# Optimization experiments

Measured on AMD Instinct MI355X. Metric: run time of the kernel, lower is better.

The kernel has to match this reference:

```python
import jax, jax.numpy as jnp
import numpy as np

B, L, C, H = 1, 256, 128, 4  # batch, seq len, c_z, n_heads
D = C // H                    # head_dim = 32


def setup_inputs() -> dict:
    key = jax.random.key(0)
    ks = jax.random.split(key, 8)
    w = lambda k, shape: jax.random.normal(k, shape, jnp.float32) * 0.02
    return {
        "pair": jax.random.normal(ks[0], (B, L, L, C), jnp.float32),
        "ln_g": jnp.ones((C,), jnp.float32),
        "ln_b": jnp.zeros((C,), jnp.float32),
        "Wq": w(ks[1], (C, C)),
        "Wk": w(ks[2], (C, C)),
        "Wv": w(ks[3], (C, C)),
        "Wbias": w(ks[4], (C, H)),
        "Wo": w(ks[5], (C, C)),
        "bo": jnp.zeros((C,), jnp.float32),
        "Wg": w(ks[6], (C, C)),
        "bg": jnp.zeros((C,), jnp.float32),
    }


def reference(pair, ln_g, ln_b, Wq, Wk, Wv, Wbias, Wo, bo, Wg, bg):
    # mode == 'starting': no transpose of pair
    # LayerNorm over c_z
    mu = jnp.mean(pair, axis=-1, keepdims=True)
    var = jnp.mean(jnp.square(pair - mu), axis=-1, keepdims=True)
    z = (pair - mu) * jax.lax.rsqrt(var + 1e-5) * ln_g + ln_b

    q = (z @ Wq).reshape(B, L, L, H, D)
    k = (z @ Wk).reshape(B, L, L, H, D)
    v = (z @ Wv).reshape(B, L, L, H, D)

    # logits: [B, H, i, j, k], scaled by 1/sqrt(head_dim)
    attn = jnp.einsum('bijhd,bikhd->bhijk', q, k) * (1.0 / np.sqrt(D).astype(np.float32))
    # pairwise additive bias: bias_proj(z) -> [B, L, L, H] -> [B, H, 1, j, k]
    bias = jnp.einsum('bjkc,ch->bhjk', z, Wbias)[:, :, None, :, :]
    attn = jax.nn.softmax(attn + bias, axis=-1)

    out = jnp.einsum('bhijk,bikhd->bijhd', attn, v).reshape(B, L, L, C)
    result = pair + jax.nn.sigmoid(pair @ Wg + bg) * (out @ Wo + bo)
    return result
```

## Files before the change

kernel.cpp:

```cpp
#include <hip/hip_runtime.h>
#include <cstdint>
#include <cstddef>

#define L_ 256
#define C_ 128
#define H_ 4
#define D_ 32
#define NP_ (L_ * L_)

typedef unsigned short u16;
typedef uint32_t u32;
typedef __attribute__((ext_vector_type(8))) short bf16x8;
typedef __attribute__((ext_vector_type(4))) float f32x4;

__device__ __forceinline__ float bflo(u32 u) { union { u32 i; float f; } v; v.i = u << 16; return v.f; }
__device__ __forceinline__ float bfhi(u32 u) { union { u32 i; float f; } v; v.i = u & 0xffff0000u; return v.f; }
__device__ __forceinline__ float b2f(u16 u) { union { u32 i; float f; } v; v.i = ((u32)u) << 16; return v.f; }
__device__ __forceinline__ u16 f2b(float f) {
    u32 x = __float_as_uint(f);
    return (u16)((x + 0x7fffu + ((x >> 16) & 1u)) >> 16);
}
__device__ __forceinline__ u32 pk2(float lo, float hi) {
    return ((u32)f2b(hi) << 16) | (u32)f2b(lo);
}
__device__ __forceinline__ bf16x8 pack8(float4 a, float4 b) {
    union { u32 u[4]; bf16x8 v; } r;
    r.u[0] = pk2(a.x, a.y); r.u[1] = pk2(a.z, a.w);
    r.u[2] = pk2(b.x, b.y); r.u[3] = pk2(b.z, b.w);
    return r.v;
}

__global__ __launch_bounds__(256) void k_prep(
    const float* __restrict__ Wq, const float* __restrict__ Wk, const float* __restrict__ Wv,
    const float* __restrict__ Wo, const float* __restrict__ Wg,
    const float* __restrict__ Wbias, u16* __restrict__ Wt, float* __restrict__ WbT)
{
    __shared__ float tile[64][65];
    const int b = blockIdx.x, t = threadIdx.x;
    if (b < 20) {
        const int mat = b >> 2, tl = b & 3, tr = tl >> 1, tc = tl & 1;
        const float* W = (mat == 0) ? Wq : (mat == 1) ? Wk : (mat == 2) ? Wv : (mat == 3) ? Wo : Wg;
        const float s = (mat == 0) ? 0.17677669529663687f : 1.f;
        const int rlo = t >> 6, col = t & 63;
        #pragma unroll
        for (int m = 0; m < 16; ++m) {
            int row = m * 4 + rlo;
            tile[row][col] = W[(size_t)(tr * 64 + row) * C_ + tc * 64 + col];
        }
        __syncthreads();
        #pragma unroll
        for (int m = 0; m < 16; ++m) {
            int n = tc * 64 + m * 4 + rlo;
            int c = tr * 64 + col;
            Wt[mat * 16384 + n * C_ + c] = f2b(tile[col][m * 4 + rlo] * s);
        }
    } else {
        #pragma unroll
        for (int m = 0; m < 2; ++m) {
            int idx = m * 256 + t;
            int h = idx >> 7, c = idx & 127;
            WbT[h * C_ + c] = Wbias[c * H_ + h];
        }
    }
}

__global__ __launch_bounds__(256) void k_lnmm(
    const float* __restrict__ pair, const float* __restrict__ ln_g, const float* __restrict__ ln_b,
    const u16* __restrict__ Wt, const float* __restrict__ WbT,
    u16* __restrict__ qh, u16* __restrict__ kh, u16* __restrict__ vh,
    u16* __restrict__ biasT)
{
    __shared__ u16 zsh[64][136];

    const int t  = threadIdx.x;
    const int p0 = blockIdx.x * 64;
    const int row = t >> 2, seg = t & 3;

    float4 xv[8];
    float sum = 0.f, ss = 0.f;
    #pragma unroll
    for (int i = 0; i < 8; ++i) {
        int c = (seg + 4 * i) * 4;
        float4 x = *(const float4*)(pair + (size_t)(p0 + row) * C_ + c);
        xv[i] = x;
        sum += x.x + x.y + x.z + x.w;
        ss  += x.x * x.x + x.y * x.y + x.z * x.z + x.w * x.w;
    }
    sum += __shfl_xor(sum, 1); sum += __shfl_xor(sum, 2);
    ss  += __shfl_xor(ss, 1);  ss  += __shfl_xor(ss, 2);
    float mu  = sum * (1.0f / C_);
    float var = ss * (1.0f / C_) - mu * mu;
    float rs  = rsqrtf(fmaxf(var, 0.f) + 1e-5f);

    #pragma unroll
    for (int i = 0; i < 8; ++i) {
        int c = (seg + 4 * i) * 4;
        float4 g4 = *(const float4*)(ln_g + c);
        float4 b4 = *(const float4*)(ln_b + c);
        float4 x  = xv[i];
        float z0 = (x.x - mu) * rs * g4.x + b4.x;
        float z1 = (x.y - mu) * rs * g4.y + b4.y;
        float z2 = (x.z - mu) * rs * g4.z + b4.z;
        float z3 = (x.w - mu) * rs * g4.w + b4.w;
        *(u32*)&zsh[row][c]     = pk2(z0, z1);
        *(u32*)&zsh[row][c + 2] = pk2(z2, z3);
    }
    __syncthreads();

    const int w    = t >> 6;
    const int l15  = t & 15;
    const int quad = (t >> 4) & 3;

    bf16x8 zf[4][4];
    #pragma unroll
    for (int jt = 0; jt < 4; ++jt)
        #pragma unroll
        for (int kc = 0; kc < 4; ++kc)
            zf[jt][kc] = *(const bf16x8*)&zsh[jt * 16 + l15][kc * 32 + quad * 8];

    #pragma unroll
    for (int k = 0; k < 6; ++k) {
        const int tt = w * 6 + k;
        const int mat = tt >> 3, mt = tt & 7;
        f32x4 acc0 = {0.f,0.f,0.f,0.f}, acc1 = acc0, acc2 = acc0, acc3 = acc0;
        #pragma unroll
        for (int kc = 0; kc < 4; ++kc) {
            bf16x8 af = *(const bf16x8*)(Wt + (size_t)tt * 2048 + (size_t)l15 * 128 + kc * 32 + quad * 8);
            acc0 = __builtin_amdgcn_mfma_f32_16x16x32_bf16(af, zf[0][kc], acc0, 0, 0, 0);
            acc1 = __builtin_amdgcn_mfma_f32_16x16x32_bf16(af, zf[1][kc], acc1, 0, 0, 0);
            acc2 = __builtin_amdgcn_mfma_f32_16x16x32_bf16(af, zf[2][kc], acc2, 0, 0, 0);
            acc3 = __builtin_amdgcn_mfma_f32_16x16x32_bf16(af, zf[3][kc], acc3, 0, 0, 0);
        }
        u16* dst = (mat == 0) ? qh : (mat == 1) ? kh : vh;
        const int hh = mt >> 1;
        const int cb = (mt & 1) * 16 + quad * 4;
        f32x4 accs[4] = {acc0, acc1, acc2, acc3};
        #pragma unroll
        for (int jt = 0; jt < 4; ++jt) {
            const int p = p0 + jt * 16 + l15;
            *(uint2*)(dst + ((size_t)hh * NP_ + p) * D_ + cb) =
                make_uint2(pk2(accs[jt][0], accs[jt][1]), pk2(accs[jt][2], accs[jt][3]));
        }
    }

    {
        float a = 0.f;
        #pragma unroll
        for (int c8 = 0; c8 < C_; c8 += 8) {
            uint4 zz = *(const uint4*)&zsh[row][c8];
            float4 wb0 = *(const float4*)(WbT + seg * C_ + c8);
            float4 wb1 = *(const float4*)(WbT + seg * C_ + c8 + 4);
            a += bflo(zz.x) * wb0.x + bfhi(zz.x) * wb0.y
               + bflo(zz.y) * wb0.z + bfhi(zz.y) * wb0.w
               + bflo(zz.z) * wb1.x + bfhi(zz.z) * wb1.y
               + bflo(zz.w) * wb1.z + bfhi(zz.w) * wb1.w;
        }
        const int p = p0 + row;
        biasT[(size_t)seg * NP_ + (p & 255) * 256 + (p >> 8)] = f2b(a);
    }
}

__global__ __launch_bounds__(256) void k_attn(
    u16* __restrict__ qh, const u16* __restrict__ kh, const u16* __restrict__ vh,
    const u16* __restrict__ biasT)
{
    __shared__ u16 Vsh[D_ * 264];
    __shared__ u16 Psh[4][16][40];

    const int t = threadIdx.x;
    const int i = blockIdx.x >> 2;
    const int h = blockIdx.x & 3;
    const int w    = t >> 6;
    const int l15  = t & 15;
    const int quad = (t >> 4) & 3;
    const int jbase = w * 64;

    const u16* Kg = kh + ((size_t)h * NP_ + i * L_) * D_;
    const u16* Vg = vh + ((size_t)h * NP_ + i * L_) * D_;
    u16*       Qg = qh + ((size_t)h * NP_ + i * L_) * D_;

    #pragma unroll
    for (int jj = 0; jj < 8; ++jj) {
        int idx = t + jj * 256;
        int r = idx >> 2, sg = idx & 3;
        union { uint4 q; u16 s[8]; } u;
        u.q = *(const uint4*)(Vg + r * D_ + sg * 8);
        #pragma unroll
        for (int m = 0; m < 8; ++m) Vsh[(sg * 8 + m) * 264 + r] = u.s[m];
    }

    bf16x8 qf[4];
    #pragma unroll
    for (int jt = 0; jt < 4; ++jt)
        qf[jt] = *(const bf16x8*)(Qg + (size_t)(jbase + jt * 16 + l15) * D_ + quad * 8);

    __syncthreads();

    const f32x4 z4 = {0.f, 0.f, 0.f, 0.f};
    f32x4 oacc[4][2];
    float psum[4][4];
    #pragma unroll
    for (int jt = 0; jt < 4; ++jt) {
        oacc[jt][0] = z4; oacc[jt][1] = z4;
        #pragma unroll
        for (int r = 0; r < 4; ++r) psum[jt][r] = 0.f;
    }

    const u16* bT = biasT + (size_t)h * NP_;

    bf16x8 kb0 = *(const bf16x8*)(Kg + (size_t)l15 * D_ + quad * 8);
    bf16x8 kb1 = *(const bf16x8*)(Kg + (size_t)(16 + l15) * D_ + quad * 8);

    for (int kc = 0; kc < 8; ++kc) {
        bf16x8 nb0, nb1;
        if (kc < 7) {
            nb0 = *(const bf16x8*)(Kg + (size_t)((kc + 1) * 32 + l15) * D_ + quad * 8);
            nb1 = *(const bf16x8*)(Kg + (size_t)((kc + 1) * 32 + 16 + l15) * D_ + quad * 8);
        }
        bf16x8 vb0 = *(const bf16x8*)&Vsh[l15 * 264 + kc * 32 + quad * 8];
        bf16x8 vb1 = *(const bf16x8*)&Vsh[(16 + l15) * 264 + kc * 32 + quad * 8];

        #pragma unroll
        for (int jt = 0; jt < 4; ++jt) {
            f32x4 s0 = __builtin_amdgcn_mfma_f32_16x16x32_bf16(qf[jt], kb0, z4, 0, 0, 0);
            f32x4 s1 = __builtin_amdgcn_mfma_f32_16x16x32_bf16(qf[jt], kb1, z4, 0, 0, 0);

            const int j0 = jbase + jt * 16 + quad * 4;
            uint2 bv0 = *(const uint2*)(bT + (size_t)(kc * 32 + l15) * L_ + j0);
            uint2 bv1 = *(const uint2*)(bT + (size_t)(kc * 32 + 16 + l15) * L_ + j0);
            const u16* b0p = (const u16*)&bv0;
            const u16* b1p = (const u16*)&bv1;

            u16 (*P)[40] = Psh[w];
            float e0[4], e1[4];
            #pragma unroll
            for (int r = 0; r < 4; ++r) {
                e0[r] = __expf(s0[r] + b2f(b0p[r]));
                e1[r] = __expf(s1[r] + b2f(b1p[r]));
                psum[jt][r] += e0[r] + e1[r];
            }
            #pragma unroll
            for (int r = 0; r < 4; ++r) {
                P[quad * 4 + r][l15]      = f2b(e0[r]);
                P[quad * 4 + r][16 + l15] = f2b(e1[r]);
            }
            bf16x8 pa = *(const bf16x8*)&P[l15][quad * 8];
            oacc[jt][0] = __builtin_amdgcn_mfma_f32_16x16x32_bf16(pa, vb0, oacc[jt][0], 0, 0, 0);
            oacc[jt][1] = __builtin_amdgcn_mfma_f32_16x16x32_bf16(pa, vb1, oacc[jt][1], 0, 0, 0);
        }
        kb0 = nb0; kb1 = nb1;
    }

    float rn[4][4];
    #pragma unroll
    for (int jt = 0; jt < 4; ++jt)
        #pragma unroll
        for (int r = 0; r < 4; ++r) {
            float s = psum[jt][r];
            s += __shfl_xor(s, 1); s += __shfl_xor(s, 2);
            s += __shfl_xor(s, 4); s += __shfl_xor(s, 8);
            rn[jt][r] = 1.f / s;
        }

    #pragma unroll
    for (int jt = 0; jt < 4; ++jt) {
        #pragma unroll
        for (int r = 0; r < 4; ++r) {
            size_t rowo = (size_t)(jbase + jt * 16 + quad * 4 + r) * D_;
            Qg[rowo + l15]      = f2b(oacc[jt][0][r] * rn[jt][r]);
            Qg[rowo + 16 + l15] = f2b(oacc[jt][1][r] * rn[jt][r]);
        }
    }
}

__global__ __launch_bounds__(256) void k_out(
    const u16* __restrict__ aoh, const float* __restrict__ pair,
    const u16* __restrict__ Wt, const float* __restrict__ bo,
    const float* __restrict__ bg, float* __restrict__ out)
{
    const int t  = threadIdx.x;
    const int p0 = blockIdx.x * 128;
    const int w    = t >> 6;
    const int l15  = t & 15;
    const int quad = (t >> 4) & 3;

    bf16x8 aof[2][4], pf[2][4];
    int prow[2];
    #pragma unroll
    for (int g = 0; g < 2; ++g) {
        prow[g] = p0 + w * 32 + g * 16 + l15;
        #pragma unroll
        for (int kc = 0; kc < 4; ++kc) {
            aof[g][kc] = *(const bf16x8*)(aoh + ((size_t)kc * NP_ + prow[g]) * D_ + quad * 8);
            const float* pp = pair + (size_t)prow[g] * C_ + kc * 32 + quad * 8;
            pf[g][kc] = pack8(*(const float4*)pp, *(const float4*)(pp + 4));
        }
    }

    const u16* WoT = Wt + 3 * 16384;
    const u16* WgT = Wt + 4 * 16384;

    #pragma unroll
    for (int nt = 0; nt < 8; ++nt) {
        f32x4 accO0 = {0.f,0.f,0.f,0.f}, accO1 = accO0, accG0 = accO0, accG1 = accO0;
        #pragma unroll
        for (int kc = 0; kc < 4; ++kc) {
            bf16x8 awo = *(const bf16x8*)(WoT + (size_t)(nt * 16 + l15) * 128 + kc * 32 + quad * 8);
            bf16x8 awg = *(const bf16x8*)(WgT + (size_t)(nt * 16 + l15) * 128 + kc * 32 + quad * 8);
            accO0 = __builtin_amdgcn_mfma_f32_16x16x32_bf16(awo, aof[0][kc], accO0, 0, 0, 0);
            accO1 = __builtin_amdgcn_mfma_f32_16x16x32_bf16(awo, aof[1][kc], accO1, 0, 0, 0);
            accG0 = __builtin_amdgcn_mfma_f32_16x16x32_bf16(awg, pf[0][kc],  accG0, 0, 0, 0);
            accG1 = __builtin_amdgcn_mfma_f32_16x16x32_bf16(awg, pf[1][kc],  accG1, 0, 0, 0);
        }
        const int ch = nt * 16 + quad * 4;
        float4 bo4 = *(const float4*)(bo + ch);
        float4 bg4 = *(const float4*)(bg + ch);
        f32x4 aO[2] = {accO0, accO1}, aG[2] = {accG0, accG1};
        #pragma unroll
        for (int g = 0; g < 2; ++g) {
            float4 pr = *(const float4*)(pair + (size_t)prow[g] * C_ + ch);
            float4 r;
            r.x = pr.x + (1.f / (1.f + __expf(-(aG[g][0] + bg4.x)))) * (aO[g][0] + bo4.x);
            r.y = pr.y + (1.f / (1.f + __expf(-(aG[g][1] + bg4.y)))) * (aO[g][1] + bo4.y);
            r.z = pr.z + (1.f / (1.f + __expf(-(aG[g][2] + bg4.z)))) * (aO[g][2] + bo4.z);
            r.w = pr.w + (1.f / (1.f + __expf(-(aG[g][3] + bg4.w)))) * (aO[g][3] + bo4.w);
            *(float4*)(out + (size_t)prow[g] * C_ + ch) = r;
        }
    }
}

extern "C" void kernel_launch(void* const* d_in, const int* in_sizes, int n_in,
                              void* d_out, int out_size, void* d_ws, size_t ws_size,
                              hipStream_t stream) {
    const float* pair  = (const float*)d_in[0];
    const float* ln_g  = (const float*)d_in[1];
    const float* ln_b  = (const float*)d_in[2];
    const float* Wq    = (const float*)d_in[3];
    const float* Wk    = (const float*)d_in[4];
    const float* Wv    = (const float*)d_in[5];
    const float* Wbias = (const float*)d_in[6];
    const float* Wo    = (const float*)d_in[7];
    const float* bo    = (const float*)d_in[8];
    const float* Wg    = (const float*)d_in[9];
    const float* bg    = (const float*)d_in[10];
    float* out = (float*)d_out;

    u16* biasT = (u16*)d_ws;
    u16* qh = biasT + (size_t)H_ * NP_;
    u16* kh = qh + (size_t)NP_ * C_;
    u16* vh = kh + (size_t)NP_ * C_;
    u16* Wt = vh + (size_t)NP_ * C_;
    float* WbT = (float*)(Wt + 5 * 16384);

    k_prep<<<21, 256, 0, stream>>>(Wq, Wk, Wv, Wo, Wg, Wbias, Wt, WbT);
    k_lnmm<<<NP_ / 64, 256, 0, stream>>>(pair, ln_g, ln_b, Wt, WbT, qh, kh, vh, biasT);
    k_attn<<<L_ * H_, 256, 0, stream>>>(qh, kh, vh, biasT);
    k_out<<<NP_ / 128, 256, 0, stream>>>(qh, pair, Wt, bo, bg, out);
}
```

Baseline: 213.7 us.

## Split attention rows across two blocks and compute transposed scores to avoid bias transpose

The attention kernel now launches twice as many blocks, each handling half of the query rows with two 16-row tiles per wave, and sets launch_bounds for higher occupancy. Scores are computed as K·Q^T so the bias can be read in natural (non-transposed) layout, and k_lnmm now writes bias without the strided transpose scatter. Probabilities are packed with v_cvt_pk_bf16_f32 and stored as vector writes to LDS, and row sums use a different cross-lane reduction. The cost is that each block reloads half of V for only half the work, and the transposed-MFMA layout and shuffle indexing must stay consistent.

Result: slower. 242.0 us (+13.2%).

```diff
diff --git a/kernel.cpp b/kernel.cpp
--- a/kernel.cpp
+++ b/kernel.cpp
@@ -68,7 +68,7 @@
     const float* __restrict__ pair, const float* __restrict__ ln_g, const float* __restrict__ ln_b,
     const u16* __restrict__ Wt, const float* __restrict__ WbT,
     u16* __restrict__ qh, u16* __restrict__ kh, u16* __restrict__ vh,
-    u16* __restrict__ biasT)
+    u16* __restrict__ biasN)
 {
     __shared__ u16 zsh[64][136];
 
@@ -156,31 +156,33 @@
                + bflo(zz.w) * wb1.z + bfhi(zz.w) * wb1.w;
         }
         const int p = p0 + row;
-        biasT[(size_t)seg * NP_ + (p & 255) * 256 + (p >> 8)] = f2b(a);
-    }
-}
-
-__global__ __launch_bounds__(256) void k_attn(
+        biasN[(size_t)seg * NP_ + p] = f2b(a);
+    }
+}
+
+__global__ __launch_bounds__(256, 6) void k_attn(
     u16* __restrict__ qh, const u16* __restrict__ kh, const u16* __restrict__ vh,
-    const u16* __restrict__ biasT)
+    const u16* __restrict__ biasN)
 {
     __shared__ u16 Vsh[D_ * 264];
     __shared__ u16 Psh[4][16][40];
 
-    const int t = threadIdx.x;
-    const int i = blockIdx.x >> 2;
-    const int h = blockIdx.x & 3;
+    const int t  = threadIdx.x;
+    const int bi = blockIdx.x;
+    const int jh = bi >> 10;
+    const int i  = (bi & 1023) >> 2;
+    const int h  = bi & 3;
     const int w    = t >> 6;
     const int l15  = t & 15;
     const int quad = (t >> 4) & 3;
-    const int jbase = w * 64;
+    const int jbase = jh * 128 + w * 32;
 
     const u16* Kg = kh + ((size_t)h * NP_ + i * L_) * D_;
     const u16* Vg = vh + ((size_t)h * NP_ + i * L_) * D_;
     u16*       Qg = qh + ((size_t)h * NP_ + i * L_) * D_;
 
     #pragma unroll
-    for (int jj = 0; jj < 8; ++jj) {
+    for (int jj = 0; jj < 4; ++jj) {
         int idx = t + jj * 256;
         int r = idx >> 2, sg = idx & 3;
         union { uint4 q; u16 s[8]; } u;
@@ -189,24 +191,19 @@
         for (int m = 0; m < 8; ++m) Vsh[(sg * 8 + m) * 264 + r] = u.s[m];
     }
 
-    bf16x8 qf[4];
-    #pragma unroll
-    for (int jt = 0; jt < 4; ++jt)
+    bf16x8 qf[2];
+    #pragma unroll
+    for (int jt = 0; jt < 2; ++jt)
         qf[jt] = *(const bf16x8*)(Qg + (size_t)(jbase + jt * 16 + l15) * D_ + quad * 8);
 
     __syncthreads();
 
     const f32x4 z4 = {0.f, 0.f, 0.f, 0.f};
-    f32x4 oacc[4][2];
-    float psum[4][4];
-    #pragma unroll
-    for (int jt = 0; jt < 4; ++jt) {
-        oacc[jt][0] = z4; oacc[jt][1] = z4;
-        #pragma unroll
-        for (int r = 0; r < 4; ++r) psum[jt][r] = 0.f;
-    }
-
-    const u16* bT = biasT + (size_t)h * NP_;
+    f32x4 oacc[2][2];
+    oacc[0][0] = z4; oacc[0][1] = z4; oacc[1][0] = z4; oacc[1][1] = z4;
+    float psum[2] = {0.f, 0.f};
+
+    const u16* bN = biasN + (size_t)h * NP_;
 
     bf16x8 kb0 = *(const bf16x8*)(Kg + (size_t)l15 * D_ + quad * 8);
     bf16x8 kb1 = *(const bf16x8*)(Kg + (size_t)(16 + l15) * D_ + quad * 8);
@@ -221,54 +218,51 @@
         bf16x8 vb1 = *(const bf16x8*)&Vsh[(16 + l15) * 264 + kc * 32 + quad * 8];
 
         #pragma unroll
-        for (int jt = 0; jt < 4; ++jt) {
-            f32x4 s0 = __builtin_amdgcn_mfma_f32_16x16x32_bf16(qf[jt], kb0, z4, 0, 0, 0);
-            f32x4 s1 = __builtin_amdgcn_mfma_f32_16x16x32_bf16(qf[jt], kb1, z4, 0, 0, 0);
-
-            const int j0 = jbase + jt * 16 + quad * 4;
-            uint2 bv0 = *(const uint2*)(bT + (size_t)(kc * 32 + l15) * L_ + j0);
-            uint2 bv1 = *(const uint2*)(bT + (size_t)(kc * 32 + 16 + l15) * L_ + j0);
+        for (int jt = 0; jt < 2; ++jt) {
+            f32x4 s0 = __builtin_amdgcn_mfma_f32_16x16x32_bf16(kb0, qf[jt], z4, 0, 0, 0);
+            f32x4 s1 = __builtin_amdgcn_mfma_f32_16x16x32_bf16(kb1, qf[jt], z4, 0, 0, 0);
+
+            const u16* bp = bN + (size_t)(jbase + jt * 16 + l15) * L_ + kc * 32 + quad * 4;
+            uint2 bv0 = *(const uint2*)bp;
+            uint2 bv1 = *(const uint2*)(bp + 16);
             const u16* b0p = (const u16*)&bv0;
             const u16* b1p = (const u16*)&bv1;
 
-            u16 (*P)[40] = Psh[w];
             float e0[4], e1[4];
             #pragma unroll
             for (int r = 0; r < 4; ++r) {
                 e0[r] = __expf(s0[r] + b2f(b0p[r]));
                 e1[r] = __expf(s1[r] + b2f(b1p[r]));
-                psum[jt][r] += e0[r] + e1[r];
+                psum[jt] += e0[r] + e1[r];
             }
-            #pragma unroll
-            for (int r = 0; r < 4; ++r) {
-                P[quad * 4 + r][l15]      = f2b(e0[r]);
-                P[quad * 4 + r][16 + l15] = f2b(e1[r]);
-            }
-            bf16x8 pa = *(const bf16x8*)&P[l15][quad * 8];
+
+            u32 w0, w1, w2, w3;
+            asm("v_cvt_pk_bf16_f32 %0, %1, %2" : "=v"(w0) : "v"(e0[0]), "v"(e0[1]));
+            asm("v_cvt_pk_bf16_f32 %0, %1, %2" : "=v"(w1) : "v"(e0[2]), "v"(e0[3]));
+            asm("v_cvt_pk_bf16_f32 %0, %1, %2" : "=v"(w2) : "v"(e1[0]), "v"(e1[1]));
+            asm("v_cvt_pk_bf16_f32 %0, %1, %2" : "=v"(w3) : "v"(e1[2]), "v"(e1[3]));
+            *(uint2*)&Psh[w][l15][quad * 4]      = make_uint2(w0, w1);
+            *(uint2*)&Psh[w][l15][16 + quad * 4] = make_uint2(w2, w3);
+
+            bf16x8 pa = *(const bf16x8*)&Psh[w][l15][quad * 8];
             oacc[jt][0] = __builtin_amdgcn_mfma_f32_16x16x32_bf16(pa, vb0, oacc[jt][0], 0, 0, 0);
             oacc[jt][1] = __builtin_amdgcn_mfma_f32_16x16x32_bf16(pa, vb1, oacc[jt][1], 0, 0, 0);
         }
         kb0 = nb0; kb1 = nb1;
     }
 
-    float rn[4][4];
-    #pragma unroll
-    for (int jt = 0; jt < 4; ++jt)
+    #pragma unroll
+    for (int jt = 0; jt < 2; ++jt) {
+        float s = psum[jt];
+        s += __shfl_xor(s, 16);
+        s += __shfl_xor(s, 32);
         #pragma unroll
         for (int r = 0; r < 4; ++r) {
-            float s = psum[jt][r];
-            s += __shfl_xor(s, 1); s += __shfl_xor(s, 2);
-            s += __shfl_xor(s, 4); s += __shfl_xor(s, 8);
-            rn[jt][r] = 1.f / s;
-        }
-
-    #pragma unroll
-    for (int jt = 0; jt < 4; ++jt) {
-        #pragma unroll
-        for (int r = 0; r < 4; ++r) {
+            float rsum = __shfl(s, quad * 20 + r);
+            float rn = 1.f / rsum;
             size_t rowo = (size_t)(jbase + jt * 16 + quad * 4 + r) * D_;
-            Qg[rowo + l15]      = f2b(oacc[jt][0][r] * rn[jt][r]);
-            Qg[rowo + 16 + l15] = f2b(oacc[jt][1][r] * rn[jt][r]);
+            Qg[rowo + l15]      = f2b(oacc[jt][0][r] * rn);
+            Qg[rowo + 16 + l15] = f2b(oacc[jt][1][r] * rn);
         }
     }
 }
@@ -345,15 +339,15 @@
     const float* bg    = (const float*)d_in[10];
     float* out = (float*)d_out;
 
-    u16* biasT = (u16*)d_ws;
-    u16* qh = biasT + (size_t)H_ * NP_;
+    u16* biasN = (u16*)d_ws;
+    u16* qh = biasN + (size_t)H_ * NP_;
     u16* kh = qh + (size_t)NP_ * C_;
     u16* vh = kh + (size_t)NP_ * C_;
     u16* Wt = vh + (size_t)NP_ * C_;
     float* WbT = (float*)(Wt + 5 * 16384);
 
     k_prep<<<21, 256, 0, stream>>>(Wq, Wk, Wv, Wo, Wg, Wbias, Wt, WbT);
-    k_lnmm<<<NP_ / 64, 256, 0, stream>>>(pair, ln_g, ln_b, Wt, WbT, qh, kh, vh, biasT);
-    k_attn<<<L_ * H_, 256, 0, stream>>>(qh, kh, vh, biasT);
+    k_lnmm<<<NP_ / 64, 256, 0, stream>>>(pair, ln_g, ln_b, Wt, WbT, qh, kh, vh, biasN);
+    k_attn<<<2 * L_ * H_, 256, 0, stream>>>(qh, kh, vh, biasN);
     k_out<<<NP_ / 128, 256, 0, stream>>>(qh, pair, Wt, bo, bg, out);
 }
```
